# Kernel tuning notes

Hardware: AMD Instinct MI355X
Metric: run time of the kernel (lower is better)

## Reference

```python
import jax, jax.numpy as jnp
import numpy as np
import math

N_PTS = 131072
K_GAUSS = 2048


def quat_to_rotmat(q):
    # q: (K,4) -> (K,3,3), normalized unit quaternion to rotation matrix
    q = q / jnp.linalg.norm(q, axis=-1, keepdims=True)
    w, x, y, z = q[:, 0], q[:, 1], q[:, 2], q[:, 3]
    R = jnp.stack([
        jnp.stack([1 - 2 * (y * y + z * z), 2 * (x * y - w * z), 2 * (x * z + w * y)], axis=-1),
        jnp.stack([2 * (x * y + w * z), 1 - 2 * (x * x + z * z), 2 * (y * z - w * x)], axis=-1),
        jnp.stack([2 * (x * z - w * y), 2 * (y * z + w * x), 1 - 2 * (x * x + y * y)], axis=-1),
    ], axis=-2)
    return R


def setup_inputs() -> dict:
    key = jax.random.key(0)
    k1, k2, k3, k4 = jax.random.split(key, 4)
    x = jax.random.normal(k1, (N_PTS, 3), dtype=jnp.float32) * 0.5
    means = jax.random.normal(k2, (K_GAUSS, 3), dtype=jnp.float32) * 0.1
    log_scales = jnp.full((K_GAUSS, 3), math.log(0.05), dtype=jnp.float32)
    # identity-ish quaternions with small perturbation (as after some training)
    q = jnp.concatenate([jnp.ones((K_GAUSS, 1), jnp.float32),
                         0.1 * jax.random.normal(k3, (K_GAUSS, 3), dtype=jnp.float32)], axis=-1)
    log_amplitudes = jnp.full((K_GAUSS,), math.log(0.1), dtype=jnp.float32) \
        + 0.1 * jax.random.normal(k4, (K_GAUSS,), dtype=jnp.float32)
    return {"x": x, "means": means, "log_scales": log_scales,
            "quaternions": q, "log_amplitudes": log_amplitudes}


def reference(x, means, log_scales, quaternions, log_amplitudes):
    # amplitudes
    amps = jnp.exp(jnp.clip(log_amplitudes, -10.0, 6.0))            # (K,)
    # covariance Sigma = R diag(s^2) R^T, regularized
    s = jnp.clip(jnp.exp(log_scales), 1e-5, 100.0)                  # (K,3)
    R = quat_to_rotmat(quaternions)                                 # (K,3,3)
    Sigma = jnp.einsum('kij,kj,klj->kil', R, s * s, R)              # (K,3,3)
    Sigma_reg = Sigma + 1e-5 * jnp.eye(3, dtype=Sigma.dtype)
    # Mahalanobis via precision A = Sigma_reg^{-1} (math-equivalent to the
    # Cholesky triangular solve in the original: mahal = diff^T A diff)
    A = jnp.linalg.inv(Sigma_reg)                                   # (K,3,3), SPD
    b = jnp.einsum('kij,kj->ki', A, means)                          # (K,3)
    c = jnp.einsum('ki,ki->k', b, means)                            # (K,)
    # mahal[n,k] = x_n^T A_k x_n - 2 x_n . b_k + c_k  (no (N,K,3) diff tensor)
    xx = x[:, :, None] * x[:, None, :]                              # (N,3,3)
    mahal = jnp.einsum('nij,kij->nk', xx, A) - 2.0 * (x @ b.T) + c[None, :]
    # weighted sum over Gaussians
    out = jnp.exp(-0.5 * mahal) @ amps                              # (N,)
    return out
```

## Files before the change

### kernel.cpp

```cpp
#include <hip/hip_runtime.h>
#include <math.h>


typedef _Float16 half8 __attribute__((ext_vector_type(8)));
typedef float    f32x4 __attribute__((ext_vector_type(4)));

#define WPB     4
#define PT      2
#define CHUNK   8
#define NBUF    2

#define EXP_SCALE 8388608.0f
#define EXP_BIAS  1064880938.0f

__device__ __forceinline__ unsigned cvt_u32_sat(float y) {
    unsigned u;
    asm("v_cvt_u32_f32 %0, %1" : "=v"(u) : "v"(y));
    return u;
}

__global__ __launch_bounds__(256) void gmf_precompute(
        const float* __restrict__ means,
        const float* __restrict__ log_scales,
        const float* __restrict__ quats,
        const float* __restrict__ log_amps,
        _Float16* __restrict__ Bf, int K, int KT) {
    int k = blockIdx.x * blockDim.x + threadIdx.x;
    if (k >= KT * 16) return;

    float gc[10];
    if (k < K) {
        float qw = quats[4*k+0], qx = quats[4*k+1], qy = quats[4*k+2], qz = quats[4*k+3];
        float qn = rsqrtf(qw*qw + qx*qx + qy*qy + qz*qz);
        qw *= qn; qx *= qn; qy *= qn; qz *= qn;

        float r00 = 1.f - 2.f*(qy*qy + qz*qz);
        float r01 = 2.f*(qx*qy - qw*qz);
        float r02 = 2.f*(qx*qz + qw*qy);
        float r10 = 2.f*(qx*qy + qw*qz);
        float r11 = 1.f - 2.f*(qx*qx + qz*qz);
        float r12 = 2.f*(qy*qz - qw*qx);
        float r20 = 2.f*(qx*qz - qw*qy);
        float r21 = 2.f*(qy*qz + qw*qx);
        float r22 = 1.f - 2.f*(qx*qx + qy*qy);

        float s0 = fminf(fmaxf(expf(log_scales[3*k+0]), 1e-5f), 100.f);
        float s1 = fminf(fmaxf(expf(log_scales[3*k+1]), 1e-5f), 100.f);
        float s2 = fminf(fmaxf(expf(log_scales[3*k+2]), 1e-5f), 100.f);
        float v0 = s0*s0, v1 = s1*s1, v2 = s2*s2;

        float S00 = r00*r00*v0 + r01*r01*v1 + r02*r02*v2 + 1e-5f;
        float S11 = r10*r10*v0 + r11*r11*v1 + r12*r12*v2 + 1e-5f;
        float S22 = r20*r20*v0 + r21*r21*v1 + r22*r22*v2 + 1e-5f;
        float S01 = r00*r10*v0 + r01*r11*v1 + r02*r12*v2;
        float S02 = r00*r20*v0 + r01*r21*v1 + r02*r22*v2;
        float S12 = r10*r20*v0 + r11*r21*v1 + r12*r22*v2;

        float c00 = S11*S22 - S12*S12;
        float c01 = S02*S12 - S01*S22;
        float c02 = S01*S12 - S02*S11;
        float det = S00*c00 + S01*c01 + S02*c02;
        float id  = 1.f/det;
        float A00 = c00*id, A01 = c01*id, A02 = c02*id;
        float A11 = (S00*S22 - S02*S02)*id;
        float A12 = (S01*S02 - S00*S12)*id;
        float A22 = (S00*S11 - S01*S01)*id;

        float m0 = means[3*k+0], m1 = means[3*k+1], m2 = means[3*k+2];
        float b0 = A00*m0 + A01*m1 + A02*m2;
        float b1 = A01*m0 + A11*m1 + A12*m2;
        float b2 = A02*m0 + A12*m1 + A22*m2;
        float cc = b0*m0 + b1*m1 + b2*m2;

        float la = fminf(fmaxf(log_amps[k], -10.f), 6.f);
        const float L2E = 1.4426950408889634f;
        const float h = -0.5f * L2E;

        gc[0] = h*A00; gc[1] = h*A11; gc[2] = h*A22;
        gc[3] = 2.f*h*A01; gc[4] = 2.f*h*A02; gc[5] = 2.f*h*A12;
        gc[6] = L2E*b0; gc[7] = L2E*b1; gc[8] = L2E*b2;
        gc[9] = h*cc + L2E*la;
    } else {
        #pragma unroll
        for (int j = 0; j < 10; ++j) gc[j] = 0.f;
        gc[9] = -60000.f;
    }

    _Float16 gh[10], gl[10];
    #pragma unroll
    for (int j = 0; j < 10; ++j) {
        gh[j] = (_Float16)gc[j];
        gl[j] = (_Float16)(gc[j] - (float)gh[j]);
    }

    int kt = k >> 4, c = k & 15;
    _Float16* dst = Bf + (size_t)kt * 64 * 8;
    #pragma unroll 32
    for (int r = 0; r < 32; ++r) {
        int lg = r >> 3, j = r & 7;
        _Float16 v = (r < 10) ? gh[r]
                   : (r < 20) ? gl[r-10]
                   : (r < 30) ? gh[r-20]
                   : (_Float16)0.f;
        dst[((size_t)lg*16 + c)*8 + j] = v;
    }
}

__device__ __forceinline__ half8 gmf_build_afr1(
        const float* __restrict__ x, int pt, int lane, int N, int PTtot) {
    int lr = lane & 15;
    int lg = lane >> 4;
    int n = pt * 16 + lr;
    float x0 = 0.f, x1 = 0.f, x2 = 0.f;
    if (pt < PTtot && n < N) { x0 = x[3*n]; x1 = x[3*n+1]; x2 = x[3*n+2]; }

    float P0 = x0*x0, P1 = x1*x1, P2 = x2*x2;
    float P3 = x0*x1, P4 = x0*x2, P5 = x1*x2;

    _Float16 h0 = (_Float16)P0, h1 = (_Float16)P1, h2 = (_Float16)P2;
    _Float16 h3 = (_Float16)P3, h4 = (_Float16)P4, h5 = (_Float16)P5;
    _Float16 h6 = (_Float16)x0, h7 = (_Float16)x1, h8 = (_Float16)x2;
    _Float16 h9 = (_Float16)1.f;
    _Float16 l0 = (_Float16)(P0 - (float)h0), l1 = (_Float16)(P1 - (float)h1);
    _Float16 l2 = (_Float16)(P2 - (float)h2), l3 = (_Float16)(P3 - (float)h3);
    _Float16 l4 = (_Float16)(P4 - (float)h4), l5 = (_Float16)(P5 - (float)h5);
    _Float16 l6 = (_Float16)(x0 - (float)h6), l7 = (_Float16)(x1 - (float)h7);
    _Float16 l8 = (_Float16)(x2 - (float)h8), l9 = (_Float16)0.f;
    _Float16 z  = (_Float16)0.f;

    half8 a;
    if      (lg == 0) a = (half8){h0,h1,h2,h3,h4,h5,h6,h7};
    else if (lg == 1) a = (half8){h8,h9,h0,h1,h2,h3,h4,h5};
    else if (lg == 2) a = (half8){h6,h7,h8,h9,l0,l1,l2,l3};
    else              a = (half8){l4,l5,l6,l7,l8,l9,z,z};
    return a;
}

#define GMF_EXPACC(CC, ACC)                                                     \
    {                                                                           \
        f32x4 y = __builtin_elementwise_fma((CC), vscale, vbias);               \
        (ACC).x += __uint_as_float(cvt_u32_sat(y.x));                           \
        (ACC).y += __uint_as_float(cvt_u32_sat(y.y));                           \
        (ACC).z += __uint_as_float(cvt_u32_sat(y.z));                           \
        (ACC).w += __uint_as_float(cvt_u32_sat(y.w));                           \
    }

__device__ __forceinline__ void gmf_epilogue1(
        f32x4 a, int pt, int lane, int N, int PTtot, float* __restrict__ out) {
    int lr = lane & 15;
    int lg = lane >> 4;
    #pragma unroll
    for (int m = 1; m <= 8; m <<= 1) {
        a.x += __shfl_xor(a.x, m);
        a.y += __shfl_xor(a.y, m);
        a.z += __shfl_xor(a.z, m);
        a.w += __shfl_xor(a.w, m);
    }
    if (lr == 0 && pt < PTtot) {
        int n0 = pt * 16 + lg * 4;
        if (n0     < N) out[n0]     = a.x;
        if (n0 + 1 < N) out[n0 + 1] = a.y;
        if (n0 + 2 < N) out[n0 + 2] = a.z;
        if (n0 + 3 < N) out[n0 + 3] = a.w;
    }
}

__global__ __launch_bounds__(256, 4) void gmf_main_ns(
        const float* __restrict__ x,
        const _Float16* __restrict__ Bfh,
        float* __restrict__ out,
        int N, int KT, int PTtot) {
    __shared__ _Float16 lbs_raw[NBUF * CHUNK * 512];

    int tid  = threadIdx.x;
    int lane = tid & 63;
    int wid  = tid >> 6;
    int pt0  = (blockIdx.x * WPB + wid) * PT;
    int pt1  = pt0 + 1;
    bool active = pt0 < PTtot;

    half8 afr0 = gmf_build_afr1(x, pt0, lane, N, PTtot);
    half8 afr1 = gmf_build_afr1(x, pt1, lane, N, PTtot);
    f32x4 acc0 = {0.f, 0.f, 0.f, 0.f};
    f32x4 acc1 = {0.f, 0.f, 0.f, 0.f};
    const f32x4 czero  = {0.f, 0.f, 0.f, 0.f};
    const f32x4 vscale = {EXP_SCALE, EXP_SCALE, EXP_SCALE, EXP_SCALE};
    const f32x4 vbias  = {EXP_BIAS,  EXP_BIAS,  EXP_BIAS,  EXP_BIAS};

    int nchunks = (KT + CHUNK - 1) / CHUNK;

#define GMF_STAGE(BUF, KBASE, NK)                                               \
    {                                                                           \
        _Pragma("unroll")                                                       \
        for (int j = 0; j < 2; ++j) {                                           \
            int tile = wid * 2 + j;                                             \
            if (tile < (NK)) {                                \
                const _Float16* src = Bfh + ((size_t)((KBASE) + tile)) * 512    \
                                          + lane * 8;                           \
                __builtin_amdgcn_global_load_lds(                               \
                    (const __attribute__((address_space(1))) void*)src,         \
                    (__attribute__((address_space(3))) void*)                   \
                        (lbs_raw + ((BUF) * CHUNK + tile) * 512 + lane * 8),    \
                    16, 0, 0);                                                  \
            }                                                                   \
        }                                                                       \
    }

    {
        int nk0 = min(CHUNK, KT);
        GMF_STAGE(0, 0, nk0)
    }
    __syncthreads();

    for (int c = 0; c < nchunks; ++c) {
        int cb = c & 1;
        int kbase = c * CHUNK;
        int nk = min(CHUNK, KT - kbase);

        if (c + 1 < nchunks) {
            int nk1 = min(CHUNK, KT - (c + 1) * CHUNK);
            GMF_STAGE(cb ^ 1, (c + 1) * CHUNK, nk1)
        }

        if (active) {
            const half8* cur = (const half8*)(lbs_raw + cb * CHUNK * 512);
            if (nk == CHUNK) {
                half8 b = cur[lane];
                f32x4 cB0 = __builtin_amdgcn_mfma_f32_16x16x32_f16(afr0, b, czero, 0, 0, 0);
                f32x4 cB1 = __builtin_amdgcn_mfma_f32_16x16x32_f16(afr1, b, czero, 0, 0, 0);
                b = cur[64 + lane];
                f32x4 cA0 = __builtin_amdgcn_mfma_f32_16x16x32_f16(afr0, b, czero, 0, 0, 0);
                f32x4 cA1 = __builtin_amdgcn_mfma_f32_16x16x32_f16(afr1, b, czero, 0, 0, 0);
                #pragma unroll
                for (int i = 2; i < CHUNK; ++i) {
                    GMF_EXPACC(cB0, acc0)
                    GMF_EXPACC(cB1, acc1)
                    cB0 = cA0; cB1 = cA1;
                    b = cur[i * 64 + lane];
                    cA0 = __builtin_amdgcn_mfma_f32_16x16x32_f16(afr0, b, czero, 0, 0, 0);
                    cA1 = __builtin_amdgcn_mfma_f32_16x16x32_f16(afr1, b, czero, 0, 0, 0);
                }
                GMF_EXPACC(cB0, acc0)
                GMF_EXPACC(cB1, acc1)
                GMF_EXPACC(cA0, acc0)
                GMF_EXPACC(cA1, acc1)
            } else {
                for (int i = 0; i < nk; ++i) {
                    half8 b = cur[i * 64 + lane];
                    f32x4 c0 = __builtin_amdgcn_mfma_f32_16x16x32_f16(afr0, b, czero, 0, 0, 0);
                    f32x4 c1 = __builtin_amdgcn_mfma_f32_16x16x32_f16(afr1, b, czero, 0, 0, 0);
                    GMF_EXPACC(c0, acc0)
                    GMF_EXPACC(c1, acc1)
                }
            }
        }

        __syncthreads();
    }

    if (active) {
        gmf_epilogue1(acc0, pt0, lane, N, PTtot, out);
        gmf_epilogue1(acc1, pt1, lane, N, PTtot, out);
    }
#undef GMF_STAGE
}

extern "C" void kernel_launch(void* const* d_in, const int* in_sizes, int n_in,
                              void* d_out, int out_size, void* d_ws, size_t ws_size,
                              hipStream_t stream) {
    const float* x          = (const float*)d_in[0];
    const float* means      = (const float*)d_in[1];
    const float* log_scales = (const float*)d_in[2];
    const float* quats      = (const float*)d_in[3];
    const float* log_amps   = (const float*)d_in[4];
    float* out = (float*)d_out;

    int K = in_sizes[4];
    int N = out_size;
    int KT = (K + 15) / 16;
    int PTtot = (N + 15) / 16;

    _Float16* Bf = (_Float16*)d_ws;

    gmf_precompute<<<(KT*16 + 255) / 256, 256, 0, stream>>>(
        means, log_scales, quats, log_amps, Bf, K, KT);

    int tiles_per_block = WPB * PT;
    int blocks = (PTtot + tiles_per_block - 1) / tiles_per_block;
    gmf_main_ns<<<blocks, 256, 0, stream>>>(x, Bf, out, N, KT, PTtot);
}
```

Baseline: 40.83 us.

## Load Gaussian tiles directly from global into registers, dropping LDS staging

Replaces the LDS double-buffered staging of precomputed Gaussian tiles (with block-wide barriers per chunk) by per-wave direct global loads into registers with a one-group software prefetch. Inactive waves exit early. This removes barrier stalls and LDS traffic but multiplies L2 reads since each wave fetches the whole table, and prefetches read slightly past the table end.

```diff
diff --git a/kernel.cpp b/kernel.cpp
--- a/kernel.cpp
+++ b/kernel.cpp
@@ -7,8 +7,6 @@
 
 #define WPB     4
 #define PT      2
-#define CHUNK   8
-#define NBUF    2
 
 #define EXP_SCALE 8388608.0f
 #define EXP_BIAS  1064880938.0f
@@ -165,19 +163,21 @@
     }
 }
 
-__global__ __launch_bounds__(256, 4) void gmf_main_ns(
+#define GMF_MF2(C0, C1, BB)                                                     \
+    C0 = __builtin_amdgcn_mfma_f32_16x16x32_f16(afr0, (BB), czero, 0, 0, 0);    \
+    C1 = __builtin_amdgcn_mfma_f32_16x16x32_f16(afr1, (BB), czero, 0, 0, 0);
+
+__global__ __launch_bounds__(256, 4) void gmf_main_gf(
         const float* __restrict__ x,
-        const _Float16* __restrict__ Bfh,
+        const half8* __restrict__ Bf,
         float* __restrict__ out,
         int N, int KT, int PTtot) {
-    __shared__ _Float16 lbs_raw[NBUF * CHUNK * 512];
-
     int tid  = threadIdx.x;
     int lane = tid & 63;
     int wid  = tid >> 6;
     int pt0  = (blockIdx.x * WPB + wid) * PT;
     int pt1  = pt0 + 1;
-    bool active = pt0 < PTtot;
+    if (pt0 >= PTtot) return;
 
     half8 afr0 = gmf_build_afr1(x, pt0, lane, N, PTtot);
     half8 afr1 = gmf_build_afr1(x, pt1, lane, N, PTtot);
@@ -187,82 +187,48 @@
     const f32x4 vscale = {EXP_SCALE, EXP_SCALE, EXP_SCALE, EXP_SCALE};
     const f32x4 vbias  = {EXP_BIAS,  EXP_BIAS,  EXP_BIAS,  EXP_BIAS};
 
-    int nchunks = (KT + CHUNK - 1) / CHUNK;
-
-#define GMF_STAGE(BUF, KBASE, NK)                                               \
-    {                                                                           \
-        _Pragma("unroll")                                                       \
-        for (int j = 0; j < 2; ++j) {                                           \
-            int tile = wid * 2 + j;                                             \
-            if (tile < (NK)) {                                \
-                const _Float16* src = Bfh + ((size_t)((KBASE) + tile)) * 512    \
-                                          + lane * 8;                           \
-                __builtin_amdgcn_global_load_lds(                               \
-                    (const __attribute__((address_space(1))) void*)src,         \
-                    (__attribute__((address_space(3))) void*)                   \
-                        (lbs_raw + ((BUF) * CHUNK + tile) * 512 + lane * 8),    \
-                    16, 0, 0);                                                  \
-            }                                                                   \
-        }                                                                       \
-    }
-
-    {
-        int nk0 = min(CHUNK, KT);
-        GMF_STAGE(0, 0, nk0)
-    }
-    __syncthreads();
-
-    for (int c = 0; c < nchunks; ++c) {
-        int cb = c & 1;
-        int kbase = c * CHUNK;
-        int nk = min(CHUNK, KT - kbase);
-
-        if (c + 1 < nchunks) {
-            int nk1 = min(CHUNK, KT - (c + 1) * CHUNK);
-            GMF_STAGE(cb ^ 1, (c + 1) * CHUNK, nk1)
-        }
-
-        if (active) {
-            const half8* cur = (const half8*)(lbs_raw + cb * CHUNK * 512);
-            if (nk == CHUNK) {
-                half8 b = cur[lane];
-                f32x4 cB0 = __builtin_amdgcn_mfma_f32_16x16x32_f16(afr0, b, czero, 0, 0, 0);
-                f32x4 cB1 = __builtin_amdgcn_mfma_f32_16x16x32_f16(afr1, b, czero, 0, 0, 0);
-                b = cur[64 + lane];
-                f32x4 cA0 = __builtin_amdgcn_mfma_f32_16x16x32_f16(afr0, b, czero, 0, 0, 0);
-                f32x4 cA1 = __builtin_amdgcn_mfma_f32_16x16x32_f16(afr1, b, czero, 0, 0, 0);
-                #pragma unroll
-                for (int i = 2; i < CHUNK; ++i) {
-                    GMF_EXPACC(cB0, acc0)
-                    GMF_EXPACC(cB1, acc1)
-                    cB0 = cA0; cB1 = cA1;
-                    b = cur[i * 64 + lane];
-                    cA0 = __builtin_amdgcn_mfma_f32_16x16x32_f16(afr0, b, czero, 0, 0, 0);
-                    cA1 = __builtin_amdgcn_mfma_f32_16x16x32_f16(afr1, b, czero, 0, 0, 0);
-                }
-                GMF_EXPACC(cB0, acc0)
-                GMF_EXPACC(cB1, acc1)
-                GMF_EXPACC(cA0, acc0)
-                GMF_EXPACC(cA1, acc1)
-            } else {
-                for (int i = 0; i < nk; ++i) {
-                    half8 b = cur[i * 64 + lane];
-                    f32x4 c0 = __builtin_amdgcn_mfma_f32_16x16x32_f16(afr0, b, czero, 0, 0, 0);
-                    f32x4 c1 = __builtin_amdgcn_mfma_f32_16x16x32_f16(afr1, b, czero, 0, 0, 0);
-                    GMF_EXPACC(c0, acc0)
-                    GMF_EXPACC(c1, acc1)
-                }
-            }
-        }
-
-        __syncthreads();
-    }
-
-    if (active) {
-        gmf_epilogue1(acc0, pt0, lane, N, PTtot, out);
-        gmf_epilogue1(acc1, pt1, lane, N, PTtot, out);
-    }
-#undef GMF_STAGE
+    const half8* bp = Bf + lane;
+
+    half8 b0 = bp[0 * 64];
+    half8 b1 = bp[1 * 64];
+    half8 b2 = bp[2 * 64];
+    half8 b3 = bp[3 * 64];
+
+    f32x4 c0, c1, d0, d1;
+    int kt = 0;
+    for (; kt + 3 < KT; kt += 4) {
+        half8 n0 = bp[(size_t)(kt + 4) * 64];
+        half8 n1 = bp[(size_t)(kt + 5) * 64];
+        half8 n2 = bp[(size_t)(kt + 6) * 64];
+        half8 n3 = bp[(size_t)(kt + 7) * 64];
+
+        GMF_MF2(c0, c1, b0)
+        GMF_MF2(d0, d1, b1)
+        GMF_EXPACC(c0, acc0) GMF_EXPACC(c1, acc1)
+        GMF_MF2(c0, c1, b2)
+        GMF_EXPACC(d0, acc0) GMF_EXPACC(d1, acc1)
+        GMF_MF2(d0, d1, b3)
+        GMF_EXPACC(c0, acc0) GMF_EXPACC(c1, acc1)
+        GMF_EXPACC(d0, acc0) GMF_EXPACC(d1, acc1)
+
+        b0 = n0; b1 = n1; b2 = n2; b3 = n3;
+    }
+    int rem = KT - kt;
+    if (rem > 0) {
+        GMF_MF2(c0, c1, b0)
+        GMF_EXPACC(c0, acc0) GMF_EXPACC(c1, acc1)
+    }
+    if (rem > 1) {
+        GMF_MF2(c0, c1, b1)
+        GMF_EXPACC(c0, acc0) GMF_EXPACC(c1, acc1)
+    }
+    if (rem > 2) {
+        GMF_MF2(c0, c1, b2)
+        GMF_EXPACC(c0, acc0) GMF_EXPACC(c1, acc1)
+    }
+
+    gmf_epilogue1(acc0, pt0, lane, N, PTtot, out);
+    gmf_epilogue1(acc1, pt1, lane, N, PTtot, out);
 }
 
 extern "C" void kernel_launch(void* const* d_in, const int* in_sizes, int n_in,
@@ -287,5 +253,5 @@
 
     int tiles_per_block = WPB * PT;
     int blocks = (PTtot + tiles_per_block - 1) / tiles_per_block;
-    gmf_main_ns<<<blocks, 256, 0, stream>>>(x, Bf, out, N, KT, PTtot);
-}
+    gmf_main_gf<<<blocks, 256, 0, stream>>>(x, (const half8*)Bf, out, N, KT, PTtot);
+}
```

Result: faster. 36.94 us (median of 2 runs) (-9.5%).
